# Performance work log

Hardware: AMD Instinct MI355X
Metric: run time of the kernel (lower is better)

## Reference

```python
import jax, jax.numpy as jnp
import numpy as np

N, M, Z_DIM = 32768, 8192, 64


def setup_inputs() -> dict:
    key = jax.random.key(0)
    kz, ke = jax.random.split(key)
    z = jax.random.normal(kz, (N, Z_DIM), dtype=jnp.float32)
    # torch: e = rand(M, z_dim) * 2 - 1  -> uniform in [-1, 1)
    e = jax.random.uniform(ke, (M, Z_DIM), dtype=jnp.float32, minval=-1.0, maxval=1.0)
    return {"z": z, "e": e}


def reference(z, e):
    # data['z'] = tanh(z)
    zt = jnp.tanh(z)                                   # (N, Z)
    # pairwise squared distance via Gram expansion:
    # ||a - b||^2 = ||a||^2 + ||b||^2 - 2 a.b  (same math as the
    # broadcasted sum((a-b)**2) without the (N, M, Z) intermediate)
    zn = jnp.sum(zt * zt, axis=1)                      # (N,)
    en = jnp.sum(e * e, axis=1)                        # (M,)
    distance = zn[:, None] + en[None, :] - 2.0 * (zt @ e.T)   # (N, M)
    # min over the batch dim N for each sample e, then mean over M
    loss = jnp.mean(jnp.min(distance, axis=0))
    return loss
```

## Files before the change

kernel.cpp:

```cpp
#include <hip/hip_runtime.h>
#include <hip/hip_bf16.h>
#include <math.h>

#define NN 32768
#define MM 8192
#define ZD 64
#define WAVES 4
#define MW 128
#define MBLK (WAVES * MW)
#define NMB (MM / MBLK)
#define NCHUNKS 64
#define CHUNK (NN / NCHUNKS)
#define NROWS 128
#define NITER (CHUNK / NROWS)
#define GRID (NMB * NCHUNKS)
#define SCALE 4294967296.0

typedef __attribute__((ext_vector_type(8))) short bf16x8;
typedef __attribute__((ext_vector_type(4))) float f32x4;

__device__ inline unsigned short f2bf(float f) {
  unsigned u = __float_as_uint(f);
  return (unsigned short)((u + 0x7fffu + ((u >> 16) & 1u)) >> 16);
}
__device__ inline float bf2f(unsigned short h) {
  return __uint_as_float(((unsigned)h) << 16);
}

__global__ __launch_bounds__(256) void prep(
    const float* __restrict__ z, const float* __restrict__ e,
    unsigned short* __restrict__ zb, float* __restrict__ zn,
    unsigned short* __restrict__ eb, float* __restrict__ en,
    unsigned* __restrict__ dmin, unsigned long long* __restrict__ acc,
    unsigned* __restrict__ cnt) {
  const int q = threadIdx.x & 7;
  if (blockIdx.x < NN / 32) {
    const int row = blockIdx.x * 32 + (threadIdx.x >> 3);
    const size_t base = (size_t)row * ZD + q * 8;
    float4 v0 = *reinterpret_cast<const float4*>(&z[base]);
    float4 v1 = *reinterpret_cast<const float4*>(&z[base + 4]);
    float in[8] = {v0.x, v0.y, v0.z, v0.w, v1.x, v1.y, v1.z, v1.w};
    unsigned short b[8];
    float s = 0.f;
#pragma unroll
    for (int i = 0; i < 8; ++i) {
      b[i] = f2bf(tanhf(in[i]));
      float r = bf2f(b[i]);
      s += r * r;
    }
    *reinterpret_cast<bf16x8*>(&zb[base]) = *reinterpret_cast<bf16x8*>(b);
    s += __shfl_xor(s, 1, 64);
    s += __shfl_xor(s, 2, 64);
    s += __shfl_xor(s, 4, 64);
    if (q == 0) zn[row] = s;
  } else {
    const int row = (blockIdx.x - NN / 32) * 32 + (threadIdx.x >> 3);
    const size_t base = (size_t)row * ZD + q * 8;
    float4 v0 = *reinterpret_cast<const float4*>(&e[base]);
    float4 v1 = *reinterpret_cast<const float4*>(&e[base + 4]);
    float in[8] = {v0.x, v0.y, v0.z, v0.w, v1.x, v1.y, v1.z, v1.w};
    unsigned short b[8];
    float s = 0.f;
#pragma unroll
    for (int i = 0; i < 8; ++i) {
      unsigned short qb = f2bf(in[i]);
      float r = bf2f(qb);
      s += r * r;
      b[i] = f2bf(-2.f * r);
    }
    *reinterpret_cast<bf16x8*>(&eb[base]) = *reinterpret_cast<bf16x8*>(b);
    s += __shfl_xor(s, 1, 64);
    s += __shfl_xor(s, 2, 64);
    s += __shfl_xor(s, 4, 64);
    if (q == 0) {
      en[row] = s;
      dmin[row] = 0xFFFFFFFFu;
    }
    if (blockIdx.x == NN / 32 && threadIdx.x == 0) {
      *acc = 0ULL;
      *cnt = 0u;
    }
  }
}

__global__ __launch_bounds__(256) void min_dist(
    const unsigned short* __restrict__ zb, const unsigned short* __restrict__ eb,
    const float* __restrict__ zn, unsigned* __restrict__ dmin) {
  __shared__ __align__(128) unsigned short zlds[2][NROWS * ZD];
  const int wg = ((blockIdx.x & 7) << 7) + (blockIdx.x >> 3);
  const int mb = wg & (NMB - 1);
  const int cb = wg >> 4;
  const int lane = threadIdx.x & 63;
  const int wv = threadIdx.x >> 6;
  const int lr = lane & 15;
  const int lg = lane >> 4;
  const int m0 = mb * MBLK + wv * MW;
  const int nb0 = cb * CHUNK;

  const int srow = lane >> 3;
  const int sslot = (lane & 7) ^ srow;
  const char* zsrc = (const char*)zb + (size_t)nb0 * 128 +
                     (wv * 32 + srow) * 128 + (sslot << 4);
  char* ldst0 = (char*)&zlds[0][0] + wv * 4096;
  char* ldst1 = (char*)&zlds[1][0] + wv * 4096;

  bf16x8 bfr[8][2];
#pragma unroll
  for (int t = 0; t < 8; ++t)
#pragma unroll
    for (int h = 0; h < 2; ++h)
      bfr[t][h] = *reinterpret_cast<const bf16x8*>(
          &eb[(size_t)(m0 + t * 16 + lr) * ZD + h * 32 + lg * 8]);

  float minv[8] = {3.4e38f, 3.4e38f, 3.4e38f, 3.4e38f,
                   3.4e38f, 3.4e38f, 3.4e38f, 3.4e38f};

  auto stage = [&](char* dst, const char* src) {
#pragma unroll
    for (int j = 0; j < 4; ++j)
      __builtin_amdgcn_global_load_lds(
          (const __attribute__((address_space(1))) unsigned int*)(src + j * 1024),
          (__attribute__((address_space(3))) unsigned int*)(dst + j * 1024),
          16, 0, 0);
  };

  const float* znp = zn + nb0;
  const int x0 = (lg * 16) ^ ((lr & 7) << 4);

  stage(ldst0, zsrc);
  zsrc += NROWS * 128;
  __syncthreads();

  for (int it = 0; it < NITER; ++it) {
    const char* lbase = (it & 1) ? (const char*)&zlds[1][0] : (const char*)&zlds[0][0];
    if (it + 1 < NITER) {
      stage((it & 1) ? ldst0 : ldst1, zsrc);
      zsrc += NROWS * 128;
    }
#pragma unroll
    for (int s = 0; s < NROWS / 16; ++s) {
      const int rb = (s * 16 + lr) * 128;
      bf16x8 a0 = *reinterpret_cast<const bf16x8*>(lbase + rb + x0);
      bf16x8 a1 = *reinterpret_cast<const bf16x8*>(lbase + rb + (x0 ^ 64));
      f32x4 znv = *reinterpret_cast<const f32x4*>(znp + s * 16 + lg * 4);
#pragma unroll
      for (int t = 0; t < 8; ++t) {
        f32x4 acc = __builtin_amdgcn_mfma_f32_16x16x32_bf16(a0, bfr[t][0], znv, 0, 0, 0);
        acc = __builtin_amdgcn_mfma_f32_16x16x32_bf16(a1, bfr[t][1], acc, 0, 0, 0);
        float x = fminf(fminf(acc[0], acc[1]), acc[2]);
        minv[t] = fminf(fminf(x, acc[3]), minv[t]);
      }
    }
    znp += NROWS;
    __syncthreads();
  }

#pragma unroll
  for (int t = 0; t < 8; ++t) {
    float v = minv[t];
    v = fminf(v, __shfl_xor(v, 16, 64));
    v = fminf(v, __shfl_xor(v, 32, 64));
    if (lg == 0) {
      unsigned bits = __float_as_uint(v);
      unsigned key = (bits & 0x80000000u) ? ~bits : (bits | 0x80000000u);
      atomicMin(&dmin[m0 + t * 16 + lr], key);
    }
  }
}

__global__ __launch_bounds__(256) void finalize(const unsigned* __restrict__ dmin,
                                                const float* __restrict__ en,
                                                unsigned long long* __restrict__ acc,
                                                unsigned* __restrict__ cnt,
                                                float* __restrict__ out) {
  const int m = blockIdx.x * 256 + threadIdx.x;
  unsigned key = dmin[m];
  unsigned bits = (key & 0x80000000u) ? (key & 0x7FFFFFFFu) : ~key;
  float mv = __uint_as_float(bits);
  double s = (double)(mv + en[m]);
  __shared__ double sred[256];
  sred[threadIdx.x] = s;
  __syncthreads();
  for (int off = 128; off > 0; off >>= 1) {
    if ((int)threadIdx.x < off) sred[threadIdx.x] += sred[threadIdx.x + off];
    __syncthreads();
  }
  if (threadIdx.x == 0) {
    unsigned long long iv = (unsigned long long)(sred[0] * SCALE + 0.5);
    atomicAdd(acc, iv);
    __threadfence();
    unsigned d = atomicAdd(cnt, 1u);
    if (d == MM / 256 - 1) {
      __threadfence();
      unsigned long long tot = atomicAdd(acc, 0ULL);
      out[0] = (float)((double)tot / SCALE / (double)MM);
    }
  }
}

extern "C" void kernel_launch(void* const* d_in, const int* in_sizes, int n_in,
                              void* d_out, int out_size, void* d_ws, size_t ws_size,
                              hipStream_t stream) {
  const float* z = (const float*)d_in[0];
  const float* e = (const float*)d_in[1];
  float* out = (float*)d_out;

  unsigned short* zb = (unsigned short*)d_ws;
  unsigned short* eb = zb + (size_t)NN * ZD;
  float* zn = (float*)(eb + (size_t)MM * ZD);
  float* en = zn + NN;
  unsigned* dmin = (unsigned*)(en + MM);
  unsigned long long* acc = (unsigned long long*)(dmin + MM);
  unsigned* cnt = (unsigned*)(acc + 1);

  prep<<<(NN + MM) / 32, 256, 0, stream>>>(z, e, zb, zn, eb, en, dmin, acc, cnt);
  min_dist<<<GRID, 256, 0, stream>>>(zb, eb, zn, dmin);
  finalize<<<MM / 256, 256, 0, stream>>>(dmin, en, acc, cnt, out);
}
```

Baseline: 51.12 us.

## Drop LDS staging; use single-wave blocks loading z fragments directly from global

The min_dist kernel moves from 4-wave workgroups that shared z tiles through double-buffered LDS to single-wave workgroups. Each wave now loads its z fragments and norms straight from global memory and prefetches them one step ahead in registers, which removes the LDS traffic and the __syncthreads barriers. The cost is that z reuse across waves now has to come from L2/L1 instead of LDS, with four times as many blocks reading the same z. Separately, tanhf in prep is replaced with an exp2/rcp approximation to cut transcendental cost.

```diff
diff --git a/kernel.cpp b/kernel.cpp
--- a/kernel.cpp
+++ b/kernel.cpp
@@ -5,14 +5,11 @@
 #define NN 32768
 #define MM 8192
 #define ZD 64
-#define WAVES 4
 #define MW 128
-#define MBLK (WAVES * MW)
-#define NMB (MM / MBLK)
+#define NMB (MM / MW)
 #define NCHUNKS 64
 #define CHUNK (NN / NCHUNKS)
-#define NROWS 128
-#define NITER (CHUNK / NROWS)
+#define NITER (CHUNK / 16)
 #define GRID (NMB * NCHUNKS)
 #define SCALE 4294967296.0
 
@@ -25,6 +22,10 @@
 }
 __device__ inline float bf2f(unsigned short h) {
   return __uint_as_float(((unsigned)h) << 16);
+}
+__device__ inline float fast_tanh(float x) {
+  float r = __builtin_amdgcn_exp2f(x * 2.8853900817779268f);
+  return fmaf(-2.f, __builtin_amdgcn_rcpf(r + 1.f), 1.f);
 }
 
 __global__ __launch_bounds__(256) void prep(
@@ -44,7 +45,7 @@
     float s = 0.f;
 #pragma unroll
     for (int i = 0; i < 8; ++i) {
-      b[i] = f2bf(tanhf(in[i]));
+      b[i] = f2bf(fast_tanh(in[i]));
       float r = bf2f(b[i]);
       s += r * r;
     }
@@ -83,26 +84,17 @@
   }
 }
 
-__global__ __launch_bounds__(256) void min_dist(
+__global__ __launch_bounds__(64) void min_dist(
     const unsigned short* __restrict__ zb, const unsigned short* __restrict__ eb,
     const float* __restrict__ zn, unsigned* __restrict__ dmin) {
-  __shared__ __align__(128) unsigned short zlds[2][NROWS * ZD];
-  const int wg = ((blockIdx.x & 7) << 7) + (blockIdx.x >> 3);
+  const int wg = ((blockIdx.x & 7) << 9) + (blockIdx.x >> 3);
   const int mb = wg & (NMB - 1);
-  const int cb = wg >> 4;
-  const int lane = threadIdx.x & 63;
-  const int wv = threadIdx.x >> 6;
+  const int cb = wg >> 6;
+  const int lane = threadIdx.x;
   const int lr = lane & 15;
   const int lg = lane >> 4;
-  const int m0 = mb * MBLK + wv * MW;
+  const int m0 = mb * MW;
   const int nb0 = cb * CHUNK;
-
-  const int srow = lane >> 3;
-  const int sslot = (lane & 7) ^ srow;
-  const char* zsrc = (const char*)zb + (size_t)nb0 * 128 +
-                     (wv * 32 + srow) * 128 + (sslot << 4);
-  char* ldst0 = (char*)&zlds[0][0] + wv * 4096;
-  char* ldst1 = (char*)&zlds[1][0] + wv * 4096;
 
   bf16x8 bfr[8][2];
 #pragma unroll
@@ -115,44 +107,30 @@
   float minv[8] = {3.4e38f, 3.4e38f, 3.4e38f, 3.4e38f,
                    3.4e38f, 3.4e38f, 3.4e38f, 3.4e38f};
 
-  auto stage = [&](char* dst, const char* src) {
+  const unsigned short* zp = zb + (size_t)(nb0 + lr) * ZD + lg * 8;
+  const float* znp = zn + nb0 + lg * 4;
+
+  bf16x8 a0 = *reinterpret_cast<const bf16x8*>(zp);
+  bf16x8 a1 = *reinterpret_cast<const bf16x8*>(zp + 32);
+  f32x4 znv = *reinterpret_cast<const f32x4*>(znp);
+
+#pragma unroll 1
+  for (int it = 0; it < NITER; ++it) {
+    zp += 16 * ZD;
+    znp += 16;
+    bf16x8 na0 = *reinterpret_cast<const bf16x8*>(zp);
+    bf16x8 na1 = *reinterpret_cast<const bf16x8*>(zp + 32);
+    f32x4 nzn = *reinterpret_cast<const f32x4*>(znp);
 #pragma unroll
-    for (int j = 0; j < 4; ++j)
-      __builtin_amdgcn_global_load_lds(
-          (const __attribute__((address_space(1))) unsigned int*)(src + j * 1024),
-          (__attribute__((address_space(3))) unsigned int*)(dst + j * 1024),
-          16, 0, 0);
-  };
-
-  const float* znp = zn + nb0;
-  const int x0 = (lg * 16) ^ ((lr & 7) << 4);
-
-  stage(ldst0, zsrc);
-  zsrc += NROWS * 128;
-  __syncthreads();
-
-  for (int it = 0; it < NITER; ++it) {
-    const char* lbase = (it & 1) ? (const char*)&zlds[1][0] : (const char*)&zlds[0][0];
-    if (it + 1 < NITER) {
-      stage((it & 1) ? ldst0 : ldst1, zsrc);
-      zsrc += NROWS * 128;
+    for (int t = 0; t < 8; ++t) {
+      f32x4 acc = __builtin_amdgcn_mfma_f32_16x16x32_bf16(a0, bfr[t][0], znv, 0, 0, 0);
+      acc = __builtin_amdgcn_mfma_f32_16x16x32_bf16(a1, bfr[t][1], acc, 0, 0, 0);
+      float x = fminf(fminf(acc[0], acc[1]), acc[2]);
+      minv[t] = fminf(fminf(x, acc[3]), minv[t]);
     }
-#pragma unroll
-    for (int s = 0; s < NROWS / 16; ++s) {
-      const int rb = (s * 16 + lr) * 128;
-      bf16x8 a0 = *reinterpret_cast<const bf16x8*>(lbase + rb + x0);
-      bf16x8 a1 = *reinterpret_cast<const bf16x8*>(lbase + rb + (x0 ^ 64));
-      f32x4 znv = *reinterpret_cast<const f32x4*>(znp + s * 16 + lg * 4);
-#pragma unroll
-      for (int t = 0; t < 8; ++t) {
-        f32x4 acc = __builtin_amdgcn_mfma_f32_16x16x32_bf16(a0, bfr[t][0], znv, 0, 0, 0);
-        acc = __builtin_amdgcn_mfma_f32_16x16x32_bf16(a1, bfr[t][1], acc, 0, 0, 0);
-        float x = fminf(fminf(acc[0], acc[1]), acc[2]);
-        minv[t] = fminf(fminf(x, acc[3]), minv[t]);
-      }
-    }
-    znp += NROWS;
-    __syncthreads();
+    a0 = na0;
+    a1 = na1;
+    znv = nzn;
   }
 
 #pragma unroll
@@ -214,6 +192,6 @@
   unsigned* cnt = (unsigned*)(acc + 1);
 
   prep<<<(NN + MM) / 32, 256, 0, stream>>>(z, e, zb, zn, eb, en, dmin, acc, cnt);
-  min_dist<<<GRID, 256, 0, stream>>>(zb, eb, zn, dmin);
+  min_dist<<<GRID, 64, 0, stream>>>(zb, eb, zn, dmin);
   finalize<<<MM / 256, 256, 0, stream>>>(dmin, en, acc, cnt, out);
 }
```

New measurement: 57.12 us. 1.12x slower.
